# Performance work log

Hardware: AMD Instinct MI355X
Metric: run time of the kernel (lower is better)

## Reference

```python
import jax, jax.numpy as jnp
import numpy as np
import math

B, N, C, H = 4, 4096, 1024, 4
D = C // H            # per-head channel dim = 256
KV_SIZE = 1024        # config.KV_sizec, used as the score scale
EPS = 1e-5            # InstanceNorm2d default eps


def setup_inputs() -> dict:
    key = jax.random.key(0)
    ks = jax.random.split(key, 9)
    f = lambda k, shape: jax.random.normal(k, shape, dtype=jnp.float32) * 0.05
    return {
        'S':   f(ks[0], (B, N, C)),
        'SKV': f(ks[1], (B, N, C)),
        'T':   f(ks[2], (B, N, C)),
        'TKV': f(ks[3], (B, N, C)),
        'Wq':  f(ks[4], (H, D, D)),   # per-head torch Linear weights [out,in]
        'Wk':  f(ks[5], (H, D, D)),
        'Wv':  f(ks[6], (H, D, D)),
        'Wout':  f(ks[7], (C, C)),
        'Woutd': f(ks[8], (C, C)),
    }


def _heads(x, W):
    # x: [B,N,C] split into H chunks of D along channels; per-head Linear (no bias).
    xh = x.reshape(B, N, H, D)
    return jnp.einsum('bnhd,hed->bhne', xh, W)  # [B,H,N,D]


def _inorm(s):
    # InstanceNorm2d (affine=False): normalize over the last two dims per (batch, head).
    m = jnp.mean(s, axis=(-2, -1), keepdims=True)
    v = jnp.var(s, axis=(-2, -1), keepdims=True)
    return (s - m) * jax.lax.rsqrt(v + EPS)


def _attend(Q, K, V, Wout):
    # Channel attention: scores [B,H,D,D], sequence dim contracted.
    scores = jnp.einsum('bhni,bhnj->bhij', Q, K) / math.sqrt(KV_SIZE)
    probs = jax.nn.softmax(_inorm(scores), axis=-1)
    ctx = jnp.einsum('bhij,bhnj->bhin', probs, V)          # [B,H,D,N]
    # permute(0,3,2,1) -> [B,N,D,H], then view merges (D,H) with head fastest.
    ctx = jnp.transpose(ctx, (0, 3, 2, 1)).reshape(B, N, C)
    return jnp.einsum('bnc,oc->bno', ctx, Wout)


def reference(S, SKV, T, TKV, Wq, Wk, Wv, Wout, Woutd):
    Q  = _heads(S,   Wq); K  = _heads(SKV, Wk); V  = _heads(SKV, Wv)
    Qd = _heads(T,   Wq); Kd = _heads(TKV, Wk); Vd = _heads(TKV, Wv)
    S2T   = _attend(Q,  Kd, Vd, Wout)   # cross: S queries, T keys/values
    T2S   = _attend(Qd, K,  V,  Woutd)  # cross: T queries, S keys/values
    S_out = _attend(Q,  K,  V,  Wout)   # self on S
    T_out = _attend(Qd, Kd, Vd, Woutd)  # self on T
    return (S_out, T2S, S2T, T_out)
```

## Files before the change

### kernel.cpp

```cpp
#include <hip/hip_runtime.h>
#include <hip/hip_bf16.h>
#include <cstdint>

using bf16 = __hip_bfloat16;
typedef __attribute__((ext_vector_type(8))) short bf16x8v;
typedef __attribute__((ext_vector_type(4))) float f32x4v;

__device__ __forceinline__ void gload_lds16(const void* g, void* l) {
  __builtin_amdgcn_global_load_lds(
      (const __attribute__((address_space(1))) void*)g,
      (__attribute__((address_space(3))) void*)l, 16, 0, 0);
}

__device__ __forceinline__ unsigned short f2bu(float x) {
  union { __hip_bfloat16 h; unsigned short u; } cv;
  cv.h = __float2bfloat16(x);
  return cv.u;
}

__device__ __forceinline__ bf16x8v cvt8(const f32x4v lo, const f32x4v hi) {
  bf16x8v t;
  t[0] = (short)f2bu(lo[0]); t[1] = (short)f2bu(lo[1]);
  t[2] = (short)f2bu(lo[2]); t[3] = (short)f2bu(lo[3]);
  t[4] = (short)f2bu(hi[0]); t[5] = (short)f2bu(hi[1]);
  t[6] = (short)f2bu(hi[2]); t[7] = (short)f2bu(hi[3]);
  return t;
}

struct GemmP {
  const void* A; const void* B; const void* A2; const void* B2; void* C;
  int K, lda, ldb, ldc, tilesN, swz;
  int d0, d1, d2;
  long long sA0, sA1, sA2, sA3;
  long long sB0, sB1, sB2, sB3;
  long long sC0, sC1, sC2, sC3;
  long long zA, zB, zC;
  float scale;
};

template<int OUT_F32, int AF32, int BF32>
__global__ __launch_bounds__(256, 4)
void gemm_bt(GemmP p)
{
  constexpr int EA = AF32 ? 4 : 2;
  constexpr int EB = BF32 ? 4 : 2;
  constexpr int ABYTES = 128 * 64 * EA;
  constexpr int BBYTES = 128 * 64 * EB;
  constexpr int SEGA = ABYTES / 4096;
  constexpr int SEGB = BBYTES / 4096;
  __shared__ __attribute__((aligned(1024))) char smem[ABYTES + BBYTES];
  const int tid  = threadIdx.x;
  const int lane = tid & 63;
  const int wid  = tid >> 6;

  int bx = blockIdx.x;
  if (p.swz) {
    const int nx = gridDim.x;
    const int q = nx >> 3, r = nx & 7;
    const int xcd = bx & 7, loc = bx >> 3;
    bx = (xcd < r ? xcd * (q + 1) : r * (q + 1) + (xcd - r) * q) + loc;
  }
  const int tn = bx % p.tilesN;
  const int tm = bx / p.tilesN;
  int idx = blockIdx.y;
  const int i0 = idx % p.d0; idx /= p.d0;
  const int i1 = idx % p.d1; idx /= p.d1;
  const int i2 = idx % p.d2;
  const int i3 = idx / p.d2;

  const char* Abase = (const char*)((p.A2 && i2) ? p.A2 : p.A);
  const char* Bbase = (const char*)((p.B2 && i2) ? p.B2 : p.B);
  const long long offA = (long long)i0*p.sA0 + (long long)i1*p.sA1 +
                         (long long)i2*p.sA2 + (long long)i3*p.sA3 +
                         (long long)blockIdx.z*p.zA;
  const long long offB = (long long)i0*p.sB0 + (long long)i1*p.sB1 +
                         (long long)i2*p.sB2 + (long long)i3*p.sB3 +
                         (long long)blockIdx.z*p.zB;
  const char* Am = Abase + offA * EA;
  const char* Bm = Bbase + offB * EB;
  const int bm = tm * 128, bn = tn * 128;

  const char* asrc[SEGA]; int aseg[SEGA];
  #pragma unroll
  for (int r = 0; r < SEGA; ++r) {
    const int oseg = (wid * SEGA + r) * 1024;
    const int o = oseg + lane * 16;
    int row, srcoff;
    if constexpr (AF32) { row = o >> 8; const int s = (o >> 4) & 15; srcoff = (s ^ (row & 15)) * 4; }
    else               { row = o >> 7; const int s = (o >> 4) & 7;  srcoff = (s ^ (row & 7)) * 8;  }
    aseg[r] = oseg;
    asrc[r] = Am + ((long long)(bm + row) * p.lda + srcoff) * EA;
  }
  const char* bsrc[SEGB]; int bseg[SEGB];
  #pragma unroll
  for (int r = 0; r < SEGB; ++r) {
    const int oseg = (wid * SEGB + r) * 1024;
    const int o = oseg + lane * 16;
    int row, srcoff;
    if constexpr (BF32) { row = o >> 8; const int s = (o >> 4) & 15; srcoff = (s ^ (row & 15)) * 4; }
    else               { row = o >> 7; const int s = (o >> 4) & 7;  srcoff = (s ^ (row & 7)) * 8;  }
    bseg[r] = oseg;
    bsrc[r] = Bm + ((long long)(bn + row) * p.ldb + srcoff) * EB;
  }

  f32x4v acc[4][4];
  #pragma unroll
  for (int i = 0; i < 4; ++i)
    #pragma unroll
    for (int j = 0; j < 4; ++j) acc[i][j] = (f32x4v){0.f, 0.f, 0.f, 0.f};

  const int wr = wid >> 1, wc = wid & 1;
  const int fr_a = wr * 64 + (lane & 15);
  const int fr_b = wc * 64 + (lane & 15);
  const int fch  = lane >> 4;

  const int nK = p.K / 64;
  for (int kt = 0; kt < nK; ++kt) {
    #pragma unroll
    for (int r = 0; r < SEGA; ++r) { gload_lds16(asrc[r], smem + aseg[r]); asrc[r] += 64 * EA; }
    #pragma unroll
    for (int r = 0; r < SEGB; ++r) { gload_lds16(bsrc[r], smem + ABYTES + bseg[r]); bsrc[r] += 64 * EB; }
    __syncthreads();
    #pragma unroll
    for (int kk = 0; kk < 2; ++kk) {
      bf16x8v a[4], b[4];
      #pragma unroll
      for (int mi = 0; mi < 4; ++mi) {
        const int row = fr_a + mi * 16;
        if constexpr (AF32) {
          const int c2 = (fch + kk * 4) * 2;
          const f32x4v lo = *(const f32x4v*)(smem + row * 256 + ((c2 ^ (row & 15)) << 4));
          const f32x4v hi = *(const f32x4v*)(smem + row * 256 + (((c2 + 1) ^ (row & 15)) << 4));
          a[mi] = cvt8(lo, hi);
        } else {
          a[mi] = *(const bf16x8v*)(smem + row * 128 + (((fch + kk * 4) ^ (row & 7)) << 4));
        }
      }
      #pragma unroll
      for (int ni = 0; ni < 4; ++ni) {
        const int row = fr_b + ni * 16;
        if constexpr (BF32) {
          const int c2 = (fch + kk * 4) * 2;
          const f32x4v lo = *(const f32x4v*)(smem + ABYTES + row * 256 + ((c2 ^ (row & 15)) << 4));
          const f32x4v hi = *(const f32x4v*)(smem + ABYTES + row * 256 + (((c2 + 1) ^ (row & 15)) << 4));
          b[ni] = cvt8(lo, hi);
        } else {
          b[ni] = *(const bf16x8v*)(smem + ABYTES + row * 128 + (((fch + kk * 4) ^ (row & 7)) << 4));
        }
      }
      #pragma unroll
      for (int mi = 0; mi < 4; ++mi)
        #pragma unroll
        for (int ni = 0; ni < 4; ++ni)
          acc[mi][ni] = __builtin_amdgcn_mfma_f32_16x16x32_bf16(a[mi], b[ni], acc[mi][ni], 0, 0, 0);
    }
    __syncthreads();
  }

  const long long coff = (long long)i0*p.sC0 + (long long)i1*p.sC1 +
                         (long long)i2*p.sC2 + (long long)i3*p.sC3 +
                         (long long)blockIdx.z*p.zC;
  const int col0 = bn + wc * 64 + (lane & 15);
  const int row0 = bm + wr * 64 + ((lane >> 4) << 2);
  if (OUT_F32) {
    float* Cp = (float*)p.C + coff;
    #pragma unroll
    for (int mi = 0; mi < 4; ++mi)
      #pragma unroll
      for (int ni = 0; ni < 4; ++ni)
        #pragma unroll
        for (int j = 0; j < 4; ++j)
          Cp[(size_t)(row0 + mi*16 + j) * p.ldc + (col0 + ni*16)] = acc[mi][ni][j] * p.scale;
  } else {
    bf16* Cp = (bf16*)p.C + coff;
    #pragma unroll
    for (int mi = 0; mi < 4; ++mi)
      #pragma unroll
      for (int ni = 0; ni < 4; ++ni)
        #pragma unroll
        for (int j = 0; j < 4; ++j)
          Cp[(size_t)(row0 + mi*16 + j) * p.ldc + (col0 + ni*16)] =
              __float2bfloat16(acc[mi][ni][j] * p.scale);
  }
}

struct G256P {
  const bf16* A; const bf16* B; void* C;
  int lda, ldb, ldc, nt, tilesN, swz;
  int d0, d1, d2;
  long long sA0, sA1, sA2, sA3;
  long long sB0, sB1, sB2, sB3;
  long long sC0, sC1, sC2, sC3;
  long long zA, zB, zC;
  float scale;
};

template<int OUT_F32>
__global__ __launch_bounds__(512, 2)
void gemm256_bt(G256P p)
{
  __shared__ __attribute__((aligned(1024))) char smem[131072];
  const int tid = threadIdx.x, lane = tid & 63, wid = tid >> 6;

  int bx = blockIdx.x;
  if (p.swz) {
    const int nx = gridDim.x;
    const int q = nx >> 3, r = nx & 7;
    const int xcd = bx & 7, loc = bx >> 3;
    bx = (xcd < r ? xcd * (q + 1) : r * (q + 1) + (xcd - r) * q) + loc;
  }
  const int tn = bx % p.tilesN, tm = bx / p.tilesN;
  int idx = blockIdx.y;
  const int i0 = idx % p.d0; idx /= p.d0;
  const int i1 = idx % p.d1; idx /= p.d1;
  const int i2 = idx % p.d2;
  const int i3 = idx / p.d2;

  const bf16* Am = p.A + ((long long)i0*p.sA0 + (long long)i1*p.sA1 +
                          (long long)i2*p.sA2 + (long long)i3*p.sA3 +
                          (long long)blockIdx.z*p.zA) + (long long)tm * 256 * p.lda;
  const bf16* Bm = p.B + ((long long)i0*p.sB0 + (long long)i1*p.sB1 +
                          (long long)i2*p.sB2 + (long long)i3*p.sB3 +
                          (long long)blockIdx.z*p.zB) + (long long)tn * 256 * p.ldb;

  const bf16 *asrc[4], *bsrc[4]; int seg[4];
  #pragma unroll
  for (int r = 0; r < 4; ++r) {
    const int oseg = (wid * 4 + r) * 1024;
    const int o = oseg + lane * 16;
    const int row = o >> 7;
    const int ch  = ((o >> 4) & 7) ^ (row & 7);
    seg[r] = oseg;
    asrc[r] = Am + (long long)row * p.lda + ch * 8;
    bsrc[r] = Bm + (long long)row * p.ldb + ch * 8;
  }

  #pragma unroll
  for (int r = 0; r < 4; ++r) {
    gload_lds16(asrc[r], smem + seg[r]);
    gload_lds16(bsrc[r], smem + 32768 + seg[r]);
    asrc[r] += 64; bsrc[r] += 64;
  }

  f32x4v acc[8][4];
  #pragma unroll
  for (int i = 0; i < 8; ++i)
    #pragma unroll
    for (int j = 0; j < 4; ++j) acc[i][j] = (f32x4v){0.f, 0.f, 0.f, 0.f};

  const int wr = wid >> 2, wc = wid & 3;
  const int rA = wr * 128 + (lane & 15);
  const int rB = wc * 64 + (lane & 15);
  const int fch = lane >> 4;

  for (int t = 0; t < p.nt; ++t) {
    const int cb = (t & 1) << 16;
    if (t + 1 < p.nt) {
      const int nb = ((t + 1) & 1) << 16;
      #pragma unroll
      for (int r = 0; r < 4; ++r) {
        gload_lds16(asrc[r], smem + nb + seg[r]);
        gload_lds16(bsrc[r], smem + nb + 32768 + seg[r]);
        asrc[r] += 64; bsrc[r] += 64;
      }
      asm volatile("s_waitcnt vmcnt(8)" ::: "memory");
    } else {
      asm volatile("s_waitcnt vmcnt(0)" ::: "memory");
    }
    __builtin_amdgcn_s_barrier();
    __builtin_amdgcn_sched_barrier(0);

    bf16x8v bfr[2][4];
    #pragma unroll
    for (int kk = 0; kk < 2; ++kk)
      #pragma unroll
      for (int ni = 0; ni < 4; ++ni) {
        const int row = rB + ni * 16;
        bfr[kk][ni] = *(const bf16x8v*)(smem + cb + 32768 + row * 128 +
                                        (((fch + kk * 4) ^ (row & 7)) << 4));
      }
    #pragma unroll
    for (int q = 0; q < 4; ++q) {
      bf16x8v afr[2][2];
      #pragma unroll
      for (int kk = 0; kk < 2; ++kk)
        #pragma unroll
        for (int mi = 0; mi < 2; ++mi) {
          const int row = rA + (q * 2 + mi) * 16;
          afr[kk][mi] = *(const bf16x8v*)(smem + cb + row * 128 +
                                          (((fch + kk * 4) ^ (row & 7)) << 4));
        }
      __builtin_amdgcn_s_setprio(1);
      #pragma unroll
      for (int kk = 0; kk < 2; ++kk)
        #pragma unroll
        for (int mi = 0; mi < 2; ++mi)
          #pragma unroll
          for (int ni = 0; ni < 4; ++ni)
            acc[q * 2 + mi][ni] = __builtin_amdgcn_mfma_f32_16x16x32_bf16(
                afr[kk][mi], bfr[kk][ni], acc[q * 2 + mi][ni], 0, 0, 0);
      __builtin_amdgcn_s_setprio(0);
    }
    __builtin_amdgcn_sched_barrier(0);
    __builtin_amdgcn_s_barrier();
  }

  const long long coff = (long long)i0*p.sC0 + (long long)i1*p.sC1 +
                         (long long)i2*p.sC2 + (long long)i3*p.sC3 +
                         (long long)blockIdx.z*p.zC;
  const int col0 = tn * 256 + wc * 64 + (lane & 15);
  const int row0 = tm * 256 + wr * 128 + ((lane >> 4) << 2);
  if (OUT_F32) {
    float* Cp = (float*)p.C + coff;
    #pragma unroll
    for (int mi = 0; mi < 8; ++mi)
      #pragma unroll
      for (int ni = 0; ni < 4; ++ni)
        #pragma unroll
        for (int j = 0; j < 4; ++j)
          Cp[(size_t)(row0 + mi*16 + j) * p.ldc + (col0 + ni*16)] = acc[mi][ni][j] * p.scale;
  } else {
    bf16* Cp = (bf16*)p.C + coff;
    #pragma unroll
    for (int mi = 0; mi < 8; ++mi)
      #pragma unroll
      for (int ni = 0; ni < 4; ++ni)
        #pragma unroll
        for (int j = 0; j < 4; ++j)
          Cp[(size_t)(row0 + mi*16 + j) * p.ldc + (col0 + ni*16)] =
              __float2bfloat16(acc[mi][ni][j] * p.scale);
  }
}

struct KVP {
  const float* X0; const float* X1;
  const bf16* Wk; const bf16* Wv;
  bf16* KT; bf16* Vc;
};

__global__ __launch_bounds__(256, 2)
void kv_fused(KVP p)
{
  __shared__ __attribute__((aligned(1024))) char smem[65536];
  const int tid = threadIdx.x, lane = tid & 63, wid = tid >> 6;
  const int jt = blockIdx.x & 1, nt = blockIdx.x >> 1;
  int idx = blockIdx.y;
  const int h = idx & 3; idx >>= 2;
  const int b = idx & 3; idx >>= 2;
  const int vi = idx;
  const float* X = (vi ? p.X1 : p.X0) + (size_t)b * 4194304 + (size_t)h * 256;
  const bf16* Wk = p.Wk + (size_t)h * 65536;
  const bf16* Wv = p.Wv + (size_t)h * 65536;
  const int n0 = nt * 128, j0 = jt * 128;

  const float* xsrc[8];
  #pragma unroll
  for (int r = 0; r < 8; ++r) {
    const int o = (wid * 8 + r) * 1024 + lane * 16;
    const int row = o >> 8, s = (o >> 4) & 15;
    xsrc[r] = X + (size_t)(n0 + row) * 1024 + (s ^ (row & 15)) * 4;
  }
  const bf16 *wksrc[4], *wvsrc[4];
  #pragma unroll
  for (int r = 0; r < 4; ++r) {
    const int o = (wid * 4 + r) * 1024 + lane * 16;
    const int row = o >> 7, s = (o >> 4) & 7;
    wksrc[r] = Wk + (size_t)(j0 + row) * 256 + (s ^ (row & 7)) * 8;
    wvsrc[r] = Wv + (size_t)(j0 + row) * 256 + (s ^ (row & 7)) * 8;
  }

  f32x4v accK[4][4], accV[4][4];
  #pragma unroll
  for (int i = 0; i < 4; ++i)
    #pragma unroll
    for (int j = 0; j < 4; ++j) {
      accK[i][j] = (f32x4v){0.f, 0.f, 0.f, 0.f};
      accV[i][j] = (f32x4v){0.f, 0.f, 0.f, 0.f};
    }

  const int wr = wid >> 1, wc = wid & 1;
  const int frW = wr * 64 + (lane & 15);
  const int frX = wc * 64 + (lane & 15);
  const int fch = lane >> 4;

  for (int kt = 0; kt < 4; ++kt) {
    #pragma unroll
    for (int r = 0; r < 8; ++r) { gload_lds16(xsrc[r], smem + (wid * 8 + r) * 1024); xsrc[r] += 64; }
    #pragma unroll
    for (int r = 0; r < 4; ++r) {
      gload_lds16(wksrc[r], smem + 32768 + (wid * 4 + r) * 1024); wksrc[r] += 64;
      gload_lds16(wvsrc[r], smem + 49152 + (wid * 4 + r) * 1024); wvsrc[r] += 64;
    }
    __syncthreads();
    #pragma unroll
    for (int kk = 0; kk < 2; ++kk) {
      bf16x8v wk[4], wv[4], x[4];
      #pragma unroll
      for (int mi = 0; mi < 4; ++mi) {
        const int row = frW + mi * 16;
        const int byo = row * 128 + (((fch + kk * 4) ^ (row & 7)) << 4);
        wk[mi] = *(const bf16x8v*)(smem + 32768 + byo);
        wv[mi] = *(const bf16x8v*)(smem + 49152 + byo);
      }
      #pragma unroll
      for (int ni = 0; ni < 4; ++ni) {
        const int row = frX + ni * 16;
        const int c2 = (fch + kk * 4) * 2;
        const f32x4v lo = *(const f32x4v*)(smem + row * 256 + ((c2 ^ (row & 15)) << 4));
        const f32x4v hi = *(const f32x4v*)(smem + row * 256 + (((c2 + 1) ^ (row & 15)) << 4));
        x[ni] = cvt8(lo, hi);
      }
      #pragma unroll
      for (int mi = 0; mi < 4; ++mi)
        #pragma unroll
        for (int ni = 0; ni < 4; ++ni) {
          accK[mi][ni] = __builtin_amdgcn_mfma_f32_16x16x32_bf16(wk[mi], x[ni], accK[mi][ni], 0, 0, 0);
          accV[ni][mi] = __builtin_amdgcn_mfma_f32_16x16x32_bf16(x[ni], wv[mi], accV[ni][mi], 0, 0, 0);
        }
    }
    __syncthreads();
  }

  const size_t kbase = (size_t)vi * 16777216 + (size_t)b * 4194304 + (size_t)h * 1048576;
  const size_t vbase = (size_t)vi * 16777216 + (size_t)b * 4194304;
  bf16* Kp = p.KT + kbase;
  bf16* Vp = p.Vc + vbase;
  const int rW = ((lane >> 4) << 2);
  #pragma unroll
  for (int mi = 0; mi < 4; ++mi)
    #pragma unroll
    for (int ni = 0; ni < 4; ++ni)
      #pragma unroll
      for (int j = 0; j < 4; ++j) {
        const int jrow = j0 + wr * 64 + mi * 16 + rW + j;
        const int ncol = n0 + wc * 64 + ni * 16 + (lane & 15);
        Kp[(size_t)jrow * 4096 + ncol] = __float2bfloat16(accK[mi][ni][j]);
        const int nrow = n0 + wc * 64 + ni * 16 + rW + j;
        const int jcol = j0 + wr * 64 + mi * 16 + (lane & 15);
        Vp[(size_t)nrow * 1024 + h * 256 + jcol] = __float2bfloat16(accV[ni][mi][j]);
      }
}

__global__ void cvt3_f32_bf16(const float* __restrict__ a0, const float* __restrict__ a1,
                              const float* __restrict__ a2,
                              unsigned short* __restrict__ out, long long ostride, int n4) {
  const int i = blockIdx.x * 256 + threadIdx.x;
  if (i >= n4) return;
  const float* src = (blockIdx.y == 0) ? a0 : (blockIdx.y == 1) ? a1 : a2;
  const float4 v = ((const float4*)src)[i];
  ushort4 o;
  o.x = f2bu(v.x); o.y = f2bu(v.y); o.z = f2bu(v.z); o.w = f2bu(v.w);
  ((ushort4*)(out + (size_t)blockIdx.y * ostride))[i] = o;
}

__global__ void wpre_kernel(const float* __restrict__ Wout, const float* __restrict__ Woutd,
                            bf16* __restrict__ Wpre) {
  const int w = blockIdx.y;
  const int flat = blockIdx.x * 256 + threadIdx.x;
  const float* Wsrc = w ? Woutd : Wout;
  const int o  = flat >> 10;
  const int c2 = flat & 1023;
  const int h  = c2 >> 8;
  const int i  = c2 & 255;
  Wpre[(size_t)w * 1048576 + flat] = __float2bfloat16(Wsrc[o * 1024 + i * 4 + h]);
}

__global__ __launch_bounds__(256)
void stats_quarter(const float* __restrict__ sp, float* __restrict__ st) {
  const int m = blockIdx.x >> 2, q = blockIdx.x & 3;
  const size_t PS = 4194304;
  const float* s = sp + (size_t)m * 65536 + (size_t)q * 16384;
  const int tid = threadIdx.x, lane = tid & 63, w = tid >> 6;

  float sum = 0.f, sq = 0.f;
  for (int i = tid; i < 4096; i += 256) {
    const float4 a = ((const float4*)s)[i];
    const float4 b = ((const float4*)(s + PS))[i];
    const float4 c = ((const float4*)(s + 2 * PS))[i];
    const float4 d = ((const float4*)(s + 3 * PS))[i];
    const float x0 = (a.x + b.x) + (c.x + d.x);
    const float x1 = (a.y + b.y) + (c.y + d.y);
    const float x2 = (a.z + b.z) + (c.z + d.z);
    const float x3 = (a.w + b.w) + (c.w + d.w);
    sum += (x0 + x1) + (x2 + x3);
    sq  += (x0 * x0 + x1 * x1) + (x2 * x2 + x3 * x3);
  }
  #pragma unroll
  for (int o = 32; o; o >>= 1) { sum += __shfl_xor(sum, o); sq += __shfl_xor(sq, o); }
  __shared__ float red[8];
  if (lane == 0) { red[w] = sum; red[4 + w] = sq; }
  __syncthreads();
  if (tid == 0) {
    st[blockIdx.x * 2]     = (red[0] + red[1]) + (red[2] + red[3]);
    st[blockIdx.x * 2 + 1] = (red[4] + red[5]) + (red[6] + red[7]);
  }
}

__global__ __launch_bounds__(256)
void softmax_t(const float* __restrict__ sp, const float* __restrict__ st,
               bf16* __restrict__ pr) {
  const int m = blockIdx.x >> 2, iq = blockIdx.x & 3;
  const size_t PS = 4194304;
  const float sum = (st[m*8+0] + st[m*8+2]) + (st[m*8+4] + st[m*8+6]);
  const float sq  = (st[m*8+1] + st[m*8+3]) + (st[m*8+5] + st[m*8+7]);
  const float mean = sum * (1.f / 65536.f);
  const float var  = sq * (1.f / 65536.f) - mean * mean;
  const float inv  = rsqrtf(var + 1e-5f);

  const int tid = threadIdx.x;
  const int i  = iq * 64 + (tid & 63);
  const int jq = tid >> 6;
  const float* cb = sp + (size_t)m * 65536 + i;

  float e[64];
  float se = 0.f;
  #pragma unroll
  for (int jj = 0; jj < 64; ++jj) {
    const size_t o = (size_t)(jq * 64 + jj) * 256;
    const float v = (cb[o] + cb[PS + o]) + (cb[2 * PS + o] + cb[3 * PS + o]);
    e[jj] = __expf((v - mean) * inv);
    se += e[jj];
  }
  __shared__ float seb[256];
  seb[tid] = se;
  __syncthreads();
  const int c = tid & 63;
  const float rvs = 1.f / ((seb[c] + seb[c + 64]) + (seb[c + 128] + seb[c + 192]));
  bf16* pc = pr + (size_t)m * 65536 + i;
  #pragma unroll
  for (int jj = 0; jj < 64; ++jj)
    pc[(size_t)(jq * 64 + jj) * 256] = __float2bfloat16(e[jj] * rvs);
}

extern "C" void kernel_launch(void* const* d_in, const int* in_sizes, int n_in,
                              void* d_out, int out_size, void* d_ws, size_t ws_size,
                              hipStream_t stream)
{
  const float* S     = (const float*)d_in[0];
  const float* SKV   = (const float*)d_in[1];
  const float* T     = (const float*)d_in[2];
  const float* TKV   = (const float*)d_in[3];
  const float* Wq    = (const float*)d_in[4];
  const float* Wk    = (const float*)d_in[5];
  const float* Wv    = (const float*)d_in[6];
  const float* Wout  = (const float*)d_in[7];
  const float* Woutd = (const float*)d_in[8];
  float* out = (float*)d_out;

  const int Hd = 4, Dd = 256;
  const long long NC  = 4096ll * 1024;
  const long long BNC = 4 * NC;
  const long long HDN = 1048576;

  char* ws = (char*)d_ws;
  size_t off = 0;
  auto alloc = [&](size_t bytes) -> void* {
    void* pp = ws + off; off += (bytes + 255) & ~(size_t)255; return pp;
  };
  bf16*  Wqb    = (bf16*)alloc((size_t)Hd * Dd * Dd * 2);
  bf16*  Wkb    = (bf16*)alloc((size_t)Hd * Dd * Dd * 2);
  bf16*  Wvb    = (bf16*)alloc((size_t)Hd * Dd * Dd * 2);
  bf16*  Wpre   = (bf16*)alloc(2ull * 1024 * 1024 * 2);
  bf16*  QT     = (bf16*)alloc(2 * BNC * 2);
  bf16*  KT     = (bf16*)alloc(2 * BNC * 2);
  bf16*  Vc     = (bf16*)alloc(2 * BNC * 2);
  float* sparts = (float*)alloc(4ull * 4194304 * 4);
  float* stats  = (float*)alloc(256ull * 2 * 4);
  bf16*  probsT = (bf16*)alloc(64ull * 65536 * 2);
  bf16*  Weff   = QT;
  if (ws_size < off) return;

  {
    const int w4 = (Hd * Dd * Dd) / 4;
    cvt3_f32_bf16<<<dim3((w4 + 255) / 256, 3), dim3(256), 0, stream>>>(
        Wq, Wk, Wv, (unsigned short*)Wqb, (long long)Hd * Dd * Dd, w4);
    wpre_kernel<<<dim3(4096, 2), dim3(256), 0, stream>>>(Wout, Woutd, Wpre);
  }

  GemmP g{};

  g.A = Wqb; g.B = S; g.A2 = nullptr; g.B2 = T; g.C = QT;
  g.K = 256; g.lda = 256; g.ldb = 1024; g.ldc = 4096; g.tilesN = 32; g.swz = 0;
  g.d0 = 4; g.d1 = 4; g.d2 = 2;
  g.sA0 = 65536; g.sA1 = 0;  g.sA2 = 0;   g.sA3 = 0;
  g.sB0 = 256;   g.sB1 = NC; g.sB2 = 0;   g.sB3 = 0;
  g.sC0 = HDN;   g.sC1 = NC; g.sC2 = BNC; g.sC3 = 0;
  g.zA = 0; g.zB = 0; g.zC = 0;
  g.scale = 1.f;
  gemm_bt<0, 0, 1><<<dim3(2 * 32, 32), dim3(256), 0, stream>>>(g);

  {
    KVP kv{SKV, TKV, Wkb, Wvb, KT, Vc};
    kv_fused<<<dim3(64, 32), dim3(256), 0, stream>>>(kv);
  }

  G256P h{};

  h.A = KT; h.B = QT; h.C = sparts;
  h.lda = 4096; h.ldb = 4096; h.ldc = 256; h.nt = 16; h.tilesN = 1; h.swz = 0;
  h.d0 = 4; h.d1 = 4; h.d2 = 2;
  h.sA0 = HDN;   h.sA1 = NC;     h.sA2 = BNC;     h.sA3 = 0;
  h.sB0 = HDN;   h.sB1 = NC;     h.sB2 = 0;       h.sB3 = BNC;
  h.sC0 = 65536; h.sC1 = 262144; h.sC2 = 1048576; h.sC3 = 2097152;
  h.zA = 1024; h.zB = 1024; h.zC = 4194304;
  h.scale = 0.03125f;
  gemm256_bt<1><<<dim3(1, 64, 4), dim3(512), 0, stream>>>(h);

  stats_quarter<<<dim3(256), dim3(256), 0, stream>>>(sparts, stats);
  softmax_t<<<dim3(256), dim3(256), 0, stream>>>(sparts, stats, probsT);

  g.A = Wpre; g.B = probsT; g.A2 = nullptr; g.B2 = nullptr; g.C = Weff;
  g.K = 256; g.lda = 1024; g.ldb = 256; g.ldc = 1024; g.tilesN = 2; g.swz = 0;
  g.d0 = 4; g.d1 = 4; g.d2 = 2;
  g.sA0 = 256;   g.sA1 = 0;       g.sA2 = 0;       g.sA3 = 1048576;
  g.sB0 = 65536; g.sB1 = 262144;  g.sB2 = 1048576; g.sB3 = 2097152;
  g.sC0 = 256;   g.sC1 = 1048576; g.sC2 = 4194304; g.sC3 = 8388608;
  g.zA = 0; g.zB = 0; g.zC = 0;
  g.scale = 1.f;
  gemm_bt<0, 0, 0><<<dim3(8 * 2, 64), dim3(256), 0, stream>>>(g);

  h.A = Vc; h.B = Weff; h.C = out;
  h.lda = 1024; h.ldb = 1024; h.ldc = 1024; h.nt = 16; h.tilesN = 4; h.swz = 1;
  h.d0 = 4; h.d1 = 2; h.d2 = 2;
  h.sA0 = NC;      h.sA1 = BNC;     h.sA2 = 0;       h.sA3 = 0;
  h.sB0 = 1048576; h.sB1 = 4194304; h.sB2 = 8388608; h.sB3 = 0;
  h.sC0 = NC;      h.sC1 = 2 * BNC; h.sC2 = BNC;     h.sC3 = 0;
  h.zA = 0; h.zB = 0; h.zC = 0;
  h.scale = 1.f;
  gemm256_bt<1><<<dim3(16 * 4, 16), dim3(512), 0, stream>>>(h);

  (void)in_sizes; (void)n_in; (void)out_size;
}
```

Measured before the change: 450.0 us.

## Restructure 256-tile GEMM into finer-grained staged pipeline with split A/B buffers

Reworks the 256x256 GEMM main loop so global-to-LDS loads of A and B are issued in halves interleaved across the four compute sub-phases. B is prefetched two k-tiles ahead and A one ahead, with separate A/B buffer regions and barriers per sub-phase. Launch bounds drop to one block per CU, giving more registers but less occupancy. This aims to hide memory latency behind MFMA work, at the cost of many more barriers per k-tile.

Result: faster. 431.8 us (-4.0%).

```diff
diff --git a/kernel.cpp b/kernel.cpp
--- a/kernel.cpp
+++ b/kernel.cpp
@@ -196,7 +196,7 @@
 };
 
 template<int OUT_F32>
-__global__ __launch_bounds__(512, 2)
+__global__ __launch_bounds__(512, 1)
 void gemm256_bt(G256P p)
 {
   __shared__ __attribute__((aligned(1024))) char smem[131072];
@@ -223,24 +223,40 @@
                           (long long)i2*p.sB2 + (long long)i3*p.sB3 +
                           (long long)blockIdx.z*p.zB) + (long long)tn * 256 * p.ldb;
 
-  const bf16 *asrc[4], *bsrc[4]; int seg[4];
-  #pragma unroll
-  for (int r = 0; r < 4; ++r) {
-    const int oseg = (wid * 4 + r) * 1024;
-    const int o = oseg + lane * 16;
-    const int row = o >> 7;
-    const int ch  = ((o >> 4) & 7) ^ (row & 7);
-    seg[r] = oseg;
-    asrc[r] = Am + (long long)row * p.lda + ch * 8;
-    bsrc[r] = Bm + (long long)row * p.ldb + ch * 8;
-  }
-
-  #pragma unroll
-  for (int r = 0; r < 4; ++r) {
-    gload_lds16(asrc[r], smem + seg[r]);
-    gload_lds16(bsrc[r], smem + 32768 + seg[r]);
-    asrc[r] += 64; bsrc[r] += 64;
-  }
+  int arow[2][2]; int ach[2][2];
+  #pragma unroll
+  for (int hh = 0; hh < 2; ++hh)
+    #pragma unroll
+    for (int l = 0; l < 2; ++l) {
+      const int seg = hh * 16 + wid * 2 + l;
+      const int o = seg * 1024 + lane * 16;
+      const int row = o >> 7;
+      arow[hh][l] = row;
+      ach[hh][l] = ((o >> 4) & 7) ^ (row & 7);
+    }
+
+  auto stageA = [&](int kt, int hh, int buf) {
+    #pragma unroll
+    for (int l = 0; l < 2; ++l) {
+      const int seg = hh * 16 + wid * 2 + l;
+      gload_lds16(Am + (long long)arow[hh][l] * p.lda + ach[hh][l] * 8 + kt * 64,
+                  smem + buf * 32768 + seg * 1024);
+    }
+  };
+  auto stageB = [&](int kt, int hh, int buf) {
+    #pragma unroll
+    for (int l = 0; l < 2; ++l) {
+      const int seg = hh * 16 + wid * 2 + l;
+      gload_lds16(Bm + (long long)arow[hh][l] * p.ldb + ach[hh][l] * 8 + kt * 64,
+                  smem + 65536 + buf * 32768 + seg * 1024);
+    }
+  };
+
+  stageA(0, 0, 0); stageA(0, 1, 0);
+  stageB(0, 0, 0); stageB(0, 1, 0);
+  if (p.nt > 1) { stageB(1, 0, 1); stageB(1, 1, 1); }
+  asm volatile("s_waitcnt vmcnt(0)" ::: "memory");
+  __builtin_amdgcn_s_barrier();
 
   f32x4v acc[8][4];
   #pragma unroll
@@ -253,56 +269,61 @@
   const int rB = wc * 64 + (lane & 15);
   const int fch = lane >> 4;
 
+  bf16x8v bfr[2][4];
+
   for (int t = 0; t < p.nt; ++t) {
-    const int cb = (t & 1) << 16;
-    if (t + 1 < p.nt) {
-      const int nb = ((t + 1) & 1) << 16;
-      #pragma unroll
-      for (int r = 0; r < 4; ++r) {
-        gload_lds16(asrc[r], smem + nb + seg[r]);
-        gload_lds16(bsrc[r], smem + nb + 32768 + seg[r]);
-        asrc[r] += 64; bsrc[r] += 64;
+    const int pb = t & 1;
+    const char* Ab = smem + pb * 32768;
+    const char* Bb = smem + 65536 + pb * 32768;
+
+    #pragma unroll
+    for (int q = 0; q < 4; ++q) {
+      if (q == 0) {
+        #pragma unroll
+        for (int kk = 0; kk < 2; ++kk)
+          #pragma unroll
+          for (int ni = 0; ni < 4; ++ni) {
+            const int row = rB + ni * 16;
+            bfr[kk][ni] = *(const bf16x8v*)(Bb + row * 128 +
+                                            (((fch + kk * 4) ^ (row & 7)) << 4));
+          }
       }
-      asm volatile("s_waitcnt vmcnt(8)" ::: "memory");
-    } else {
-      asm volatile("s_waitcnt vmcnt(0)" ::: "memory");
-    }
-    __builtin_amdgcn_s_barrier();
-    __builtin_amdgcn_sched_barrier(0);
-
-    bf16x8v bfr[2][4];
-    #pragma unroll
-    for (int kk = 0; kk < 2; ++kk)
-      #pragma unroll
-      for (int ni = 0; ni < 4; ++ni) {
-        const int row = rB + ni * 16;
-        bfr[kk][ni] = *(const bf16x8v*)(smem + cb + 32768 + row * 128 +
-                                        (((fch + kk * 4) ^ (row & 7)) << 4));
+      bf16x8v afr[2][2];
+      #pragma unroll
+      for (int kk = 0; kk < 2; ++kk)
+        #pragma unroll
+        for (int s = 0; s < 2; ++s) {
+          const int row = rA + (q * 2 + s) * 16;
+          afr[kk][s] = *(const bf16x8v*)(Ab + row * 128 +
+                                         (((fch + kk * 4) ^ (row & 7)) << 4));
+        }
+      if (q == 0 && t + 1 < p.nt) stageA(t + 1, 0, pb ^ 1);
+      if (q == 1 && t + 1 < p.nt) stageA(t + 1, 1, pb ^ 1);
+      if (q == 2 && t + 2 < p.nt) stageB(t + 2, 0, pb);
+      if (q == 3) {
+        if (t + 2 < p.nt) {
+          stageB(t + 2, 1, pb);
+          asm volatile("s_waitcnt vmcnt(4)" ::: "memory");
+        } else {
+          asm volatile("s_waitcnt vmcnt(0)" ::: "memory");
+        }
       }
-    #pragma unroll
-    for (int q = 0; q < 4; ++q) {
-      bf16x8v afr[2][2];
+      __builtin_amdgcn_s_barrier();
+      asm volatile("s_waitcnt lgkmcnt(0)" ::: "memory");
+      __builtin_amdgcn_sched_barrier(0);
+      __builtin_amdgcn_s_setprio(1);
       #pragma unroll
       for (int kk = 0; kk < 2; ++kk)
         #pragma unroll
-        for (int mi = 0; mi < 2; ++mi) {
-          const int row = rA + (q * 2 + mi) * 16;
-          afr[kk][mi] = *(const bf16x8v*)(smem + cb + row * 128 +
-                                          (((fch + kk * 4) ^ (row & 7)) << 4));
-        }
-      __builtin_amdgcn_s_setprio(1);
-      #pragma unroll
-      for (int kk = 0; kk < 2; ++kk)
-        #pragma unroll
-        for (int mi = 0; mi < 2; ++mi)
+        for (int s = 0; s < 2; ++s)
           #pragma unroll
           for (int ni = 0; ni < 4; ++ni)
-            acc[q * 2 + mi][ni] = __builtin_amdgcn_mfma_f32_16x16x32_bf16(
-                afr[kk][mi], bfr[kk][ni], acc[q * 2 + mi][ni], 0, 0, 0);
+            acc[q * 2 + s][ni] = __builtin_amdgcn_mfma_f32_16x16x32_bf16(
+                afr[kk][s], bfr[kk][ni], acc[q * 2 + s][ni], 0, 0, 0);
       __builtin_amdgcn_s_setprio(0);
-    }
-    __builtin_amdgcn_sched_barrier(0);
-    __builtin_amdgcn_s_barrier();
+      __builtin_amdgcn_sched_barrier(0);
+      __builtin_amdgcn_s_barrier();
+    }
   }
 
   const long long coff = (long long)i0*p.sC0 + (long long)i1*p.sC1 +
```
